# Kernel optimization log

Measured on AMD Instinct MI355X. Metric: run time of the kernel, lower is better.

## Reference

```python
import jax, jax.numpy as jnp
import numpy as np

B, S, E, H, K, V = 2, 2048, 2048, 16, 128, 128
EPS = 1e-5


def _rotate(x, cos, sin):
    half = K // 2
    swapped = jnp.concatenate((x[..., half:], x[..., :half]), axis=-1)
    return cos * x + sin * swapped


def setup_inputs() -> dict:
    key = jax.random.key(0)
    k1, k2, k3 = jax.random.split(key, 3)
    embeddings = jax.random.normal(k1, (B, S, E), jnp.float32)
    pos = jnp.arange(S, dtype=jnp.float32)[:, None]
    inv_freq = 1.0 / (10000.0 ** (jnp.arange(0, K, 2, dtype=jnp.float32) / K))
    ang = pos * inv_freq[None, :]
    ang = jnp.concatenate((ang, ang), axis=-1)
    cosb = jnp.cos(ang)[None, None, :, :]
    sinb = jnp.sin(ang)[None, None, :, :]
    cos_buffer = jnp.stack((cosb, cosb))
    sin_buffer = jnp.stack((sinb, sinb))
    causal_buffer = jnp.tril(jnp.ones((S, S), dtype=bool))[None, None]
    w_norm = jnp.ones((E,), jnp.float32)
    w_qkv = jax.random.normal(k2, (E, 2 * K * H + V * H), jnp.float32) * 0.02
    w_out = jax.random.normal(k3, (H * V, E), jnp.float32) * 0.02
    return dict(embeddings=embeddings, cos_buffer=cos_buffer, sin_buffer=sin_buffer,
                causal_buffer=causal_buffer, w_norm=w_norm, w_qkv=w_qkv, w_out=w_out)


def reference(embeddings, cos_buffer, sin_buffer, causal_buffer, w_norm, w_qkv, w_out):
    ms = jnp.mean(embeddings * embeddings, axis=-1, keepdims=True)
    normed = embeddings * jax.lax.rsqrt(ms + EPS) * w_norm
    qkv = normed @ w_qkv
    ks = K * H
    q = qkv[..., :ks].reshape(B, S, H, K).transpose(0, 2, 1, 3)
    k = qkv[..., ks:2 * ks].reshape(B, S, H, K).transpose(0, 2, 1, 3)
    v = qkv[..., 2 * ks:].reshape(B, S, H, V).transpose(0, 2, 1, 3)
    present_k, present_v = k, v
    q = _rotate(q, cos_buffer[0], sin_buffer[0])
    k = _rotate(k, cos_buffer[1], sin_buffer[1])
    scores = jnp.einsum('bhqk,bhsk->bhqs', q, k) / np.float32(np.sqrt(K))
    scores = jnp.where(causal_buffer, scores, -jnp.inf)
    attn = jax.nn.softmax(scores, axis=-1)
    out = jnp.einsum('bhqs,bhsv->bhqv', attn, v)
    out = out.transpose(0, 2, 1, 3).reshape(B, S, H * V) @ w_out
    return embeddings + out, present_k, present_v
```

## Files before the change

kernel.cpp:

```cpp
#include <hip/hip_runtime.h>

typedef unsigned short u16;
typedef unsigned int   u32;
typedef short bf16x8 __attribute__((ext_vector_type(8)));
typedef float f32x4  __attribute__((ext_vector_type(4)));
typedef float f4     __attribute__((ext_vector_type(4)));
typedef u16   u16x4  __attribute__((ext_vector_type(4)));
typedef u16   u16x8  __attribute__((ext_vector_type(8)));
typedef u32   u32x2  __attribute__((ext_vector_type(2)));

__device__ __forceinline__ u16 f2bf(float x) {
  u32 u = __float_as_uint(x);
  u += 0x7fff + ((u >> 16) & 1);
  return (u16)(u >> 16);
}
__device__ __forceinline__ float bf2f(u16 h) {
  return __uint_as_float(((u32)h) << 16);
}
__device__ __forceinline__ void gload16(const void* g, void* l) {
  __builtin_amdgcn_global_load_lds((const __attribute__((address_space(1))) u32*)g,
                                   (__attribute__((address_space(3))) u32*)l, 16, 0, 0);
}
__device__ __forceinline__ f32x4 mfma16(bf16x8 a, bf16x8 b, f32x4 c) {
  return __builtin_amdgcn_mfma_f32_16x16x32_bf16(a, b, c, 0, 0, 0);
}

__global__ __launch_bounds__(256) void k_rmsnorm(const float* __restrict__ x,
                                                 const float* __restrict__ w,
                                                 u16* __restrict__ out) {
  const int row = blockIdx.x, tid = threadIdx.x;
  const float* xr = x + (size_t)row * 2048;
  f4 a = *(const f4*)&xr[tid * 8];
  f4 b = *(const f4*)&xr[tid * 8 + 4];
  float ss = a[0]*a[0]+a[1]*a[1]+a[2]*a[2]+a[3]*a[3]+b[0]*b[0]+b[1]*b[1]+b[2]*b[2]+b[3]*b[3];
#pragma unroll
  for (int off = 32; off > 0; off >>= 1) ss += __shfl_xor(ss, off);
  __shared__ float red[4];
  if ((tid & 63) == 0) red[tid >> 6] = ss;
  __syncthreads();
  ss = red[0] + red[1] + red[2] + red[3];
  const float sc = rsqrtf(ss * (1.0f / 2048.0f) + 1e-5f);
  f4 wa = *(const f4*)&w[tid * 8];
  f4 wb = *(const f4*)&w[tid * 8 + 4];
  u16x8 o;
#pragma unroll
  for (int i = 0; i < 4; ++i) o[i] = f2bf(a[i] * sc * wa[i]);
#pragma unroll
  for (int i = 0; i < 4; ++i) o[4 + i] = f2bf(b[i] * sc * wb[i]);
  *(u16x8*)&out[(size_t)row * 2048 + tid * 8] = o;
}

__global__ __launch_bounds__(256) void k_transpose_cvt(const float* __restrict__ src,
                                                       u16* __restrict__ dst,
                                                       int R, int C) {
  __shared__ float t[32][33];
  const int tid = threadIdx.x;
  const size_t zoff = (size_t)blockIdx.z * (size_t)R * (size_t)C;
  src += zoff; dst += zoff;
  const int r0 = blockIdx.y * 32, c0 = blockIdx.x * 32;
  const int rr = tid >> 3, cc = (tid & 7) * 4;
  f4 v = *(const f4*)&src[(size_t)(r0 + rr) * C + c0 + cc];
  t[rr][cc] = v[0]; t[rr][cc + 1] = v[1]; t[rr][cc + 2] = v[2]; t[rr][cc + 3] = v[3];
  __syncthreads();
  const int oc = tid >> 3, orr = (tid & 7) * 4;
  u16x4 o;
#pragma unroll
  for (int k = 0; k < 4; ++k) o[k] = f2bf(t[orr + k][oc]);
  *(u16x4*)&dst[(size_t)(c0 + oc) * R + r0 + orr] = o;
}

__device__ __forceinline__ void stage128(const u16* __restrict__ A,
                                         const u16* __restrict__ Bt,
                                         int m0, int n0, int kt,
                                         u16* dA, u16* dB, int tid) {
#pragma unroll
  for (int p = 0; p < 4; ++p) {
    int c = p * 256 + tid;
    int row = c >> 3, ch = c & 7, gch = ch ^ (row & 7);
    gload16(&A[(size_t)(m0 + row) * 2048 + kt * 64 + gch * 8], &dA[c * 8]);
    gload16(&Bt[(size_t)(n0 + row) * 2048 + kt * 64 + gch * 8], &dB[c * 8]);
  }
}

template <int EPI>
__global__ __launch_bounds__(256) void k_gemm128(
    const u16* __restrict__ A, const u16* __restrict__ Bt,
    u16* __restrict__ q_pre, float* __restrict__ outK, float* __restrict__ outV,
    const float* __restrict__ emb, float* __restrict__ out0,
    u16* __restrict__ vtf) {
  constexpr int NT = 32;
  __shared__ __align__(16) u16 lA[2][128 * 64];
  __shared__ __align__(16) u16 lB[2][128 * 64];
  const int tid = threadIdx.x;
  const int lane = tid & 63;
  const int w = tid >> 6;
  const int wr = w >> 1, wc = w & 1;
  const int g = lane >> 4, c15 = lane & 15;
  const int m0 = blockIdx.y * 128, n0 = blockIdx.x * 128;
  f32x4 acc[4][4] = {};

  stage128(A, Bt, m0, n0, 0, lA[0], lB[0], tid);
  asm volatile("s_waitcnt vmcnt(0)" ::: "memory");
  __builtin_amdgcn_s_barrier();

  for (int kt = 0; kt < NT; ++kt) {
    const int cur = kt & 1;
    if (kt + 1 < NT)
      stage128(A, Bt, m0, n0, kt + 1, lA[cur ^ 1], lB[cur ^ 1], tid);

#pragma unroll
    for (int ks = 0; ks < 2; ++ks) {
      bf16x8 af[4], bfr[4];
#pragma unroll
      for (int i = 0; i < 4; ++i) {
        int row = wr * 64 + i * 16 + c15;
        int chn = (ks * 4 + g) ^ (row & 7);
        af[i] = *(const bf16x8*)&lA[cur][row * 64 + chn * 8];
      }
#pragma unroll
      for (int j = 0; j < 4; ++j) {
        int row = wc * 64 + j * 16 + c15;
        int chn = (ks * 4 + g) ^ (row & 7);
        bfr[j] = *(const bf16x8*)&lB[cur][row * 64 + chn * 8];
      }
      __builtin_amdgcn_s_setprio(1);
#pragma unroll
      for (int i = 0; i < 4; ++i)
#pragma unroll
        for (int j = 0; j < 4; ++j)
          acc[i][j] = mfma16(af[i], bfr[j], acc[i][j]);
      __builtin_amdgcn_s_setprio(0);
    }
    asm volatile("s_waitcnt vmcnt(0)" ::: "memory");
    __builtin_amdgcn_s_barrier();
  }

  const int rb = m0 + wr * 64 + g * 4;
  const int cb = wc * 64 + c15;
  if (EPI == 0) {
    const int sec = n0 >> 11;
    const int h = (n0 & 2047) >> 7;
#pragma unroll
    for (int i = 0; i < 4; ++i)
#pragma unroll
      for (int j = 0; j < 4; ++j) {
        const int d = cb + j * 16;
        const int mb = rb + i * 16;
        const int b_ = mb >> 11, s0 = mb & 2047;
#pragma unroll
        for (int r = 0; r < 4; ++r) {
          size_t o = ((size_t)(b_ * 16 + h) * 2048 + (s0 + r)) * 128 + d;
          float val = acc[i][j][r];
          if (sec == 0)      q_pre[o] = f2bf(val);
          else if (sec == 1) outK[o] = val;
          else               outV[o] = val;
        }
        if (sec == 2 && vtf != nullptr) {
          u16x4 vt;
#pragma unroll
          for (int r = 0; r < 4; ++r) vt[r] = f2bf(acc[i][j][r]);
          *(u16x4*)&vtf[((size_t)(b_ * 16 + h) * 128 + d) * 2048 + s0] = vt;
        }
      }
  } else {
#pragma unroll
    for (int i = 0; i < 4; ++i)
#pragma unroll
      for (int j = 0; j < 4; ++j)
#pragma unroll
        for (int r = 0; r < 4; ++r) {
          int mm = rb + i * 16 + r;
          int nn = n0 + cb + j * 16;
          size_t o = (size_t)mm * 2048 + nn;
          out0[o] = acc[i][j][r] + emb[o];
        }
  }
}

__global__ __launch_bounds__(256) void k_rope(const u16* __restrict__ qp,
                                              const float* __restrict__ kp,
                                              const float* __restrict__ cosb,
                                              const float* __restrict__ sinb,
                                              u16* __restrict__ qr, u16* __restrict__ kr) {
  const int gid = blockIdx.x * 256 + threadIdx.x;
  const int row = gid >> 4;
  const int d0 = (gid & 15) * 4;
  const int s = row & 2047;
  const float SC = 0.08838834764831845f;
  const float* c1 = cosb + (size_t)s * 128;
  const float* s1 = sinb + (size_t)s * 128;
  const float* c2 = c1 + 262144;
  const float* s2 = s1 + 262144;
  const size_t base = (size_t)row * 128;
  f4 cl = *(const f4*)&c1[d0], ch = *(const f4*)&c1[d0 + 64];
  f4 sl = *(const f4*)&s1[d0], sh = *(const f4*)&s1[d0 + 64];
  {
    u16x4 xl = *(const u16x4*)&qp[base + d0];
    u16x4 xh = *(const u16x4*)&qp[base + d0 + 64];
    u16x4 ol, oh;
#pragma unroll
    for (int i = 0; i < 4; ++i) {
      float lo = bf2f(xl[i]), hi = bf2f(xh[i]);
      ol[i] = f2bf((cl[i] * lo + sl[i] * hi) * SC);
      oh[i] = f2bf((ch[i] * hi + sh[i] * lo) * SC);
    }
    *(u16x4*)&qr[base + d0] = ol;
    *(u16x4*)&qr[base + d0 + 64] = oh;
  }
  {
    f4 c2l = *(const f4*)&c2[d0], c2h = *(const f4*)&c2[d0 + 64];
    f4 s2l = *(const f4*)&s2[d0], s2h = *(const f4*)&s2[d0 + 64];
    f4 xl = *(const f4*)&kp[base + d0];
    f4 xh = *(const f4*)&kp[base + d0 + 64];
    u16x4 ol, oh;
#pragma unroll
    for (int i = 0; i < 4; ++i) {
      ol[i] = f2bf(c2l[i] * xl[i] + s2l[i] * xh[i]);
      oh[i] = f2bf(c2h[i] * xh[i] + s2h[i] * xl[i]);
    }
    *(u16x4*)&kr[base + d0] = ol;
    *(u16x4*)&kr[base + d0 + 64] = oh;
  }
}

__device__ __forceinline__ void stage_kv(const u16* kb, const u16* vb, int kv0,
                                         u16* dK, u16* dV, int tid) {
#pragma unroll
  for (int p = 0; p < 4; ++p) {
    int c = p * 256 + tid;
    { int row = c >> 4, ch = c & 15, gch = ch ^ (row & 7);
      gload16(&kb[(size_t)(kv0 + row) * 128 + gch * 8], &dK[c * 8]); }
    { int row = c >> 3, ch = c & 7, gch = ch ^ (row & 7);
      gload16(&vb[(size_t)row * 2048 + kv0 + gch * 8], &dV[c * 8]); }
  }
}

__global__ __launch_bounds__(256) void k_attn(const u16* __restrict__ q_rot,
                                              const u16* __restrict__ k_rot,
                                              const u16* __restrict__ v_t,
                                              u16* __restrict__ attn_o) {
  const int bh = blockIdx.y;
  const int b = bh >> 4, h = bh & 15;
  const int tid = threadIdx.x, w = tid >> 6, lane = tid & 63;
  const int g = lane >> 4, c15 = lane & 15;
  __shared__ __align__(16) u16 lK[2][64 * 128];
  __shared__ __align__(16) u16 lV[2][128 * 64];
  __shared__ __align__(16) u16 lP[4][16 * 64];

  const u16* qb = q_rot + (size_t)bh * 2048 * 128;
  const u16* kb = k_rot + (size_t)bh * 2048 * 128;
  const u16* vb = v_t + (size_t)bh * 128 * 2048;
  const float L2E = 1.442695040888963f;
  const float SHIFT = 11.541560327111707f;

  for (int halfp = 0; halfp < 2; ++halfp) {
    const int qt = halfp ? (int)blockIdx.x : 31 - (int)blockIdx.x;
    const int q0 = qt * 64;
    const int nt = qt + 1;

    bf16x8 qf[4];
    const int qrow = q0 + w * 16 + c15;
#pragma unroll
    for (int f = 0; f < 4; ++f)
      qf[f] = *(const bf16x8*)&qb[(size_t)qrow * 128 + f * 32 + g * 8];

    f32x4 O[8];
#pragma unroll
    for (int i = 0; i < 8; ++i) O[i] = {0.f, 0.f, 0.f, 0.f};
    float lsum = 0.0f;

    stage_kv(kb, vb, 0, &lK[0][0], &lV[0][0], tid);
    asm volatile("s_waitcnt vmcnt(0)" ::: "memory");
    __builtin_amdgcn_s_barrier();

    int cur = 0;
    for (int t = 0; t < nt; ++t) {
      if (t + 1 < nt)
        stage_kv(kb, vb, (t + 1) * 64, &lK[cur ^ 1][0], &lV[cur ^ 1][0], tid);

      const int kv0 = t * 64;
      f32x4 S[4];
#pragma unroll
      for (int n = 0; n < 4; ++n) S[n] = {0.f, 0.f, 0.f, 0.f};
      __builtin_amdgcn_s_setprio(1);
#pragma unroll
      for (int ks = 0; ks < 4; ++ks) {
#pragma unroll
        for (int n = 0; n < 4; ++n) {
          int row = n * 16 + c15;
          int chn = (ks * 4 + g) ^ (row & 7);
          bf16x8 kf = *(const bf16x8*)&lK[cur][row * 128 + chn * 8];
          S[n] = mfma16(kf, qf[ks], S[n]);
        }
      }
      __builtin_amdgcn_s_setprio(0);

      if (t == nt - 1) {
#pragma unroll
        for (int n = 0; n < 4; ++n)
#pragma unroll
          for (int r = 0; r < 4; ++r)
            if (kv0 + n * 16 + g * 4 + r > qrow) S[n][r] = -1e30f;
      }
#pragma unroll
      for (int n = 0; n < 4; ++n) {
        float p0 = exp2f(__builtin_fmaf(S[n][0], L2E, -SHIFT));
        float p1 = exp2f(__builtin_fmaf(S[n][1], L2E, -SHIFT));
        float p2 = exp2f(__builtin_fmaf(S[n][2], L2E, -SHIFT));
        float p3 = exp2f(__builtin_fmaf(S[n][3], L2E, -SHIFT));
        lsum += (p0 + p1) + (p2 + p3);
        u32x2 pw;
        pw[0] = (u32)f2bf(p0) | ((u32)f2bf(p1) << 16);
        pw[1] = (u32)f2bf(p2) | ((u32)f2bf(p3) << 16);
        int chunk = n * 2 + (g >> 1);
        int eoff = c15 * 64 + ((chunk ^ (c15 & 7)) << 3) + ((g & 1) << 2);
        *(u32x2*)&lP[w][eoff] = pw;
      }

      __builtin_amdgcn_s_setprio(1);
#pragma unroll
      for (int ks = 0; ks < 2; ++ks) {
        int ch2 = (ks * 4 + g) ^ (c15 & 7);
        bf16x8 pf = *(const bf16x8*)&lP[w][c15 * 64 + ch2 * 8];
#pragma unroll
        for (int nn = 0; nn < 8; ++nn) {
          int row = nn * 16 + c15;
          int chn = (ks * 4 + g) ^ (row & 7);
          bf16x8 vf = *(const bf16x8*)&lV[cur][row * 64 + chn * 8];
          O[nn] = mfma16(pf, vf, O[nn]);
        }
      }
      __builtin_amdgcn_s_setprio(0);

      asm volatile("s_waitcnt vmcnt(0)" ::: "memory");
      __builtin_amdgcn_s_barrier();
      cur ^= 1;
    }

    lsum += __shfl_xor(lsum, 16);
    lsum += __shfl_xor(lsum, 32);
    const float inv = 1.0f / lsum;
    float invr[4];
#pragma unroll
    for (int r = 0; r < 4; ++r)
      invr[r] = __shfl(inv, g * 4 + r);
#pragma unroll
    for (int nn = 0; nn < 8; ++nn)
#pragma unroll
      for (int r = 0; r < 4; ++r) {
        int s_ = q0 + w * 16 + g * 4 + r;
        int col = h * 128 + nn * 16 + c15;
        attn_o[(size_t)(b * 2048 + s_) * 2048 + col] = f2bf(O[nn][r] * invr[r]);
      }
  }
}

extern "C" void kernel_launch(void* const* d_in, const int* in_sizes, int n_in,
                              void* d_out, int out_size, void* d_ws, size_t ws_size,
                              hipStream_t stream) {
  const float* emb    = (const float*)d_in[0];
  const float* cosb   = (const float*)d_in[1];
  const float* sinb   = (const float*)d_in[2];
  const float* w_norm = (const float*)d_in[4];
  const float* w_qkv  = (const float*)d_in[5];
  const float* w_out  = (const float*)d_in[6];

  float* out0 = (float*)d_out;
  float* outK = out0 + 8388608;
  float* outV = out0 + 16777216;

  char* ws = (char*)d_ws;
  u16* normed = (u16*)(ws + 0);
  u16* wqkvT  = (u16*)(ws + 16777216);
  u16* woutT  = (u16*)(ws + 41943040);
  u16* q_pre  = (u16*)(ws + 50331648);
  u16* q_rot  = (u16*)(ws + 67108864);
  u16* k_rot  = (u16*)(ws + 83886080);
  u16* attn_o = normed;

  const bool fuse_vt = ws_size >= (size_t)117440512;
  u16* v_t = fuse_vt ? (u16*)(ws + 100663296) : wqkvT;

  k_rmsnorm<<<4096, 256, 0, stream>>>(emb, w_norm, normed);
  k_transpose_cvt<<<dim3(192, 64, 1), 256, 0, stream>>>(w_qkv, wqkvT, 2048, 6144);
  k_transpose_cvt<<<dim3(64, 64, 1), 256, 0, stream>>>(w_out, woutT, 2048, 2048);
  k_gemm128<0><<<dim3(48, 32), 256, 0, stream>>>(normed, wqkvT, q_pre, outK, outV,
                                                 nullptr, nullptr,
                                                 fuse_vt ? v_t : nullptr);
  k_rope<<<4096, 256, 0, stream>>>(q_pre, outK, cosb, sinb, q_rot, k_rot);
  if (!fuse_vt)
    k_transpose_cvt<<<dim3(4, 64, 32), 256, 0, stream>>>(outV, v_t, 2048, 128);
  k_attn<<<dim3(16, 32), 256, 0, stream>>>(q_rot, k_rot, v_t, attn_o);
  k_gemm128<1><<<dim3(16, 32), 256, 0, stream>>>(attn_o, woutT, nullptr, nullptr, nullptr,
                                                 emb, out0, nullptr);
}
```

Measured before the change: 298.0 us.

## Fuse RoPE into QKV GEMM epilogue via shared-memory tile staging

Removes the separate RoPE kernel. The QKV GEMM epilogue now writes Q/K tiles as bf16 into reused shared memory, then applies the rotation (and the query scale) and writes q_rot/k_rot directly. This avoids writing and re-reading the q_pre intermediate and one kernel launch. In exchange it adds a barrier and some scalar cos/sin global loads in the GEMM epilogue. The rounding order changes slightly, because K is now rounded to bf16 before rotation instead of rotated in fp32.

```diff
diff --git a/kernel.cpp b/kernel.cpp
--- a/kernel.cpp
+++ b/kernel.cpp
@@ -85,12 +85,12 @@
 template <int EPI>
 __global__ __launch_bounds__(256) void k_gemm128(
     const u16* __restrict__ A, const u16* __restrict__ Bt,
-    u16* __restrict__ q_pre, float* __restrict__ outK, float* __restrict__ outV,
+    float* __restrict__ outK, float* __restrict__ outV,
     const float* __restrict__ emb, float* __restrict__ out0,
-    u16* __restrict__ vtf) {
+    u16* __restrict__ vtf, u16* __restrict__ qr, u16* __restrict__ kr,
+    const float* __restrict__ cosb, const float* __restrict__ sinb) {
   constexpr int NT = 32;
-  __shared__ __align__(16) u16 lA[2][128 * 64];
-  __shared__ __align__(16) u16 lB[2][128 * 64];
+  __shared__ __align__(16) u16 sm[4][128 * 64];
   const int tid = threadIdx.x;
   const int lane = tid & 63;
   const int w = tid >> 6;
@@ -99,14 +99,14 @@
   const int m0 = blockIdx.y * 128, n0 = blockIdx.x * 128;
   f32x4 acc[4][4] = {};
 
-  stage128(A, Bt, m0, n0, 0, lA[0], lB[0], tid);
+  stage128(A, Bt, m0, n0, 0, sm[0], sm[2], tid);
   asm volatile("s_waitcnt vmcnt(0)" ::: "memory");
   __builtin_amdgcn_s_barrier();
 
   for (int kt = 0; kt < NT; ++kt) {
     const int cur = kt & 1;
     if (kt + 1 < NT)
-      stage128(A, Bt, m0, n0, kt + 1, lA[cur ^ 1], lB[cur ^ 1], tid);
+      stage128(A, Bt, m0, n0, kt + 1, sm[cur ^ 1], sm[2 + (cur ^ 1)], tid);
 
 #pragma unroll
     for (int ks = 0; ks < 2; ++ks) {
@@ -115,13 +115,13 @@
       for (int i = 0; i < 4; ++i) {
         int row = wr * 64 + i * 16 + c15;
         int chn = (ks * 4 + g) ^ (row & 7);
-        af[i] = *(const bf16x8*)&lA[cur][row * 64 + chn * 8];
+        af[i] = *(const bf16x8*)&sm[cur][row * 64 + chn * 8];
       }
 #pragma unroll
       for (int j = 0; j < 4; ++j) {
         int row = wc * 64 + j * 16 + c15;
         int chn = (ks * 4 + g) ^ (row & 7);
-        bfr[j] = *(const bf16x8*)&lB[cur][row * 64 + chn * 8];
+        bfr[j] = *(const bf16x8*)&sm[2 + cur][row * 64 + chn * 8];
       }
       __builtin_amdgcn_s_setprio(1);
 #pragma unroll
@@ -140,6 +140,7 @@
   if (EPI == 0) {
     const int sec = n0 >> 11;
     const int h = (n0 & 2047) >> 7;
+    u16* tile = (u16*)sm;
 #pragma unroll
     for (int i = 0; i < 4; ++i)
 #pragma unroll
@@ -147,21 +148,54 @@
         const int d = cb + j * 16;
         const int mb = rb + i * 16;
         const int b_ = mb >> 11, s0 = mb & 2047;
-#pragma unroll
-        for (int r = 0; r < 4; ++r) {
-          size_t o = ((size_t)(b_ * 16 + h) * 2048 + (s0 + r)) * 128 + d;
-          float val = acc[i][j][r];
-          if (sec == 0)      q_pre[o] = f2bf(val);
-          else if (sec == 1) outK[o] = val;
-          else               outV[o] = val;
+        if (sec == 2) {
+          u16x4 vt;
+#pragma unroll
+          for (int r = 0; r < 4; ++r) {
+            size_t o = ((size_t)(b_ * 16 + h) * 2048 + (s0 + r)) * 128 + d;
+            outV[o] = acc[i][j][r];
+            vt[r] = f2bf(acc[i][j][r]);
+          }
+          if (vtf != nullptr)
+            *(u16x4*)&vtf[((size_t)(b_ * 16 + h) * 128 + d) * 2048 + s0] = vt;
+        } else {
+#pragma unroll
+          for (int r = 0; r < 4; ++r) {
+            const int sl = wr * 64 + i * 16 + g * 4 + r;
+            if (sec == 1) {
+              size_t o = ((size_t)(b_ * 16 + h) * 2048 + (s0 + r)) * 128 + d;
+              outK[o] = acc[i][j][r];
+            }
+            tile[sl * 128 + (d ^ ((sl & 15) << 1))] = f2bf(acc[i][j][r]);
+          }
         }
-        if (sec == 2 && vtf != nullptr) {
-          u16x4 vt;
-#pragma unroll
-          for (int r = 0; r < 4; ++r) vt[r] = f2bf(acc[i][j][r]);
-          *(u16x4*)&vtf[((size_t)(b_ * 16 + h) * 128 + d) * 2048 + s0] = vt;
-        }
-      }
+      }
+    if (sec < 2) {
+      __syncthreads();
+      const float* cA = (sec == 0) ? cosb : cosb + 262144;
+      const float* sA = (sec == 0) ? sinb : sinb + 262144;
+      u16* dst = (sec == 0) ? qr : kr;
+      const float scale = (sec == 0) ? 0.08838834764831845f : 1.0f;
+      const int b_ = m0 >> 11;
+      const int sbase = m0 & 2047;
+      const int dcol = tid & 63;
+      const int srow0 = (tid >> 6) * 32;
+      u16* drow = dst + (size_t)(b_ * 16 + h) * 2048 * 128;
+#pragma unroll 4
+      for (int si = 0; si < 32; ++si) {
+        const int sl = srow0 + si;
+        const int sg = sbase + sl;
+        const int xw = (sl & 15) << 1;
+        float cl = cA[(size_t)sg * 128 + dcol];
+        float ch = cA[(size_t)sg * 128 + 64 + dcol];
+        float sl_ = sA[(size_t)sg * 128 + dcol];
+        float sh = sA[(size_t)sg * 128 + 64 + dcol];
+        float lo = bf2f(tile[sl * 128 + (dcol ^ xw)]);
+        float hi = bf2f(tile[sl * 128 + ((dcol ^ xw) + 64)]);
+        drow[(size_t)sg * 128 + dcol]      = f2bf((cl * lo + sl_ * hi) * scale);
+        drow[(size_t)sg * 128 + 64 + dcol] = f2bf((ch * hi + sh * lo) * scale);
+      }
+    }
   } else {
 #pragma unroll
     for (int i = 0; i < 4; ++i)
@@ -174,52 +208,6 @@
           size_t o = (size_t)mm * 2048 + nn;
           out0[o] = acc[i][j][r] + emb[o];
         }
-  }
-}
-
-__global__ __launch_bounds__(256) void k_rope(const u16* __restrict__ qp,
-                                              const float* __restrict__ kp,
-                                              const float* __restrict__ cosb,
-                                              const float* __restrict__ sinb,
-                                              u16* __restrict__ qr, u16* __restrict__ kr) {
-  const int gid = blockIdx.x * 256 + threadIdx.x;
-  const int row = gid >> 4;
-  const int d0 = (gid & 15) * 4;
-  const int s = row & 2047;
-  const float SC = 0.08838834764831845f;
-  const float* c1 = cosb + (size_t)s * 128;
-  const float* s1 = sinb + (size_t)s * 128;
-  const float* c2 = c1 + 262144;
-  const float* s2 = s1 + 262144;
-  const size_t base = (size_t)row * 128;
-  f4 cl = *(const f4*)&c1[d0], ch = *(const f4*)&c1[d0 + 64];
-  f4 sl = *(const f4*)&s1[d0], sh = *(const f4*)&s1[d0 + 64];
-  {
-    u16x4 xl = *(const u16x4*)&qp[base + d0];
-    u16x4 xh = *(const u16x4*)&qp[base + d0 + 64];
-    u16x4 ol, oh;
-#pragma unroll
-    for (int i = 0; i < 4; ++i) {
-      float lo = bf2f(xl[i]), hi = bf2f(xh[i]);
-      ol[i] = f2bf((cl[i] * lo + sl[i] * hi) * SC);
-      oh[i] = f2bf((ch[i] * hi + sh[i] * lo) * SC);
-    }
-    *(u16x4*)&qr[base + d0] = ol;
-    *(u16x4*)&qr[base + d0 + 64] = oh;
-  }
-  {
-    f4 c2l = *(const f4*)&c2[d0], c2h = *(const f4*)&c2[d0 + 64];
-    f4 s2l = *(const f4*)&s2[d0], s2h = *(const f4*)&s2[d0 + 64];
-    f4 xl = *(const f4*)&kp[base + d0];
-    f4 xh = *(const f4*)&kp[base + d0 + 64];
-    u16x4 ol, oh;
-#pragma unroll
-    for (int i = 0; i < 4; ++i) {
-      ol[i] = f2bf(c2l[i] * xl[i] + s2l[i] * xh[i]);
-      oh[i] = f2bf(c2h[i] * xh[i] + s2h[i] * xl[i]);
-    }
-    *(u16x4*)&kr[base + d0] = ol;
-    *(u16x4*)&kr[base + d0 + 64] = oh;
   }
 }
 
@@ -373,7 +361,6 @@
   u16* normed = (u16*)(ws + 0);
   u16* wqkvT  = (u16*)(ws + 16777216);
   u16* woutT  = (u16*)(ws + 41943040);
-  u16* q_pre  = (u16*)(ws + 50331648);
   u16* q_rot  = (u16*)(ws + 67108864);
   u16* k_rot  = (u16*)(ws + 83886080);
   u16* attn_o = normed;
@@ -384,13 +371,14 @@
   k_rmsnorm<<<4096, 256, 0, stream>>>(emb, w_norm, normed);
   k_transpose_cvt<<<dim3(192, 64, 1), 256, 0, stream>>>(w_qkv, wqkvT, 2048, 6144);
   k_transpose_cvt<<<dim3(64, 64, 1), 256, 0, stream>>>(w_out, woutT, 2048, 2048);
-  k_gemm128<0><<<dim3(48, 32), 256, 0, stream>>>(normed, wqkvT, q_pre, outK, outV,
+  k_gemm128<0><<<dim3(48, 32), 256, 0, stream>>>(normed, wqkvT, outK, outV,
                                                  nullptr, nullptr,
-                                                 fuse_vt ? v_t : nullptr);
-  k_rope<<<4096, 256, 0, stream>>>(q_pre, outK, cosb, sinb, q_rot, k_rot);
+                                                 fuse_vt ? v_t : nullptr,
+                                                 q_rot, k_rot, cosb, sinb);
   if (!fuse_vt)
     k_transpose_cvt<<<dim3(4, 64, 32), 256, 0, stream>>>(outV, v_t, 2048, 128);
   k_attn<<<dim3(16, 32), 256, 0, stream>>>(q_rot, k_rot, v_t, attn_o);
-  k_gemm128<1><<<dim3(16, 32), 256, 0, stream>>>(attn_o, woutT, nullptr, nullptr, nullptr,
-                                                 emb, out0, nullptr);
-}
+  k_gemm128<1><<<dim3(16, 32), 256, 0, stream>>>(attn_o, woutT, nullptr, nullptr,
+                                                 emb, out0, nullptr,
+                                                 nullptr, nullptr, nullptr, nullptr);
+}
```

New measurement: 280.1 us. 1.06x faster.
